# Performance work log

Measured on AMD Instinct MI355X. Metric: run time of the kernel, lower is better.

Reference implementation:

```python
import math
import jax, jax.numpy as jnp
import numpy as np

# ---- config (from ModelConfig) ----
HIDDEN = 2880
HEAD_DIM = 64
N_HEADS = 64
N_KV = 8
Q_MULT = N_HEADS // N_KV  # 8
SLIDING_WINDOW = 128      # left context; causal windowed attention
ROPE_BASE = 150000.0
ROPE_SCALE = 32.0
NTK_ALPHA = 1.0
NTK_BETA = 32.0
INIT_CTX = 4096
RMS_EPS = 1e-5
SM_SCALE = 1.0 / math.sqrt(HEAD_DIM)
Q_DIM = N_HEADS * HEAD_DIM   # 4096
KV_DIM = N_KV * HEAD_DIM     # 512
QKV_DIM = Q_DIM + 2 * KV_DIM # 5120
B, T = 1, 2048


def _rope_cos_sin(n_tokens):
    """YaRN-scaled rotary cache, per RotaryEmbedding._compute_concentration_and_inv_freq."""
    d_half = HEAD_DIM // 2
    freq = ROPE_BASE ** (jnp.arange(0, HEAD_DIM, 2, dtype=jnp.float32) / HEAD_DIM)
    concentration = 0.1 * math.log(ROPE_SCALE) + 1.0
    low = d_half * math.log(INIT_CTX / (NTK_BETA * 2 * math.pi)) / math.log(ROPE_BASE)
    high = d_half * math.log(INIT_CTX / (NTK_ALPHA * 2 * math.pi)) / math.log(ROPE_BASE)
    interpolation = 1.0 / (ROPE_SCALE * freq)
    extrapolation = 1.0 / freq
    ramp = (jnp.arange(d_half, dtype=jnp.float32) - low) / (high - low)
    mask = 1.0 - jnp.clip(ramp, 0.0, 1.0)
    inv_freq = interpolation * (1.0 - mask) + extrapolation * mask
    pos = jnp.arange(n_tokens, dtype=jnp.float32)
    angles = pos[:, None] * inv_freq[None, :]  # [t, d/2]
    return jnp.cos(angles) * concentration, jnp.sin(angles) * concentration


def _apply_rope(x, cos, sin):
    """Interleaved RoPE (matches _apply_rotary_emb). x: [b, t, ..., d]."""
    shape = x.shape
    n_mid = x.ndim - 3  # dims between token axis and feature axis
    c = cos.reshape((1, shape[1]) + (1,) * n_mid + (shape[-1] // 2,))
    s = sin.reshape((1, shape[1]) + (1,) * n_mid + (shape[-1] // 2,))
    x1 = x[..., ::2]
    x2 = x[..., 1::2]
    o1 = x1 * c - x2 * s
    o2 = x2 * c + x1 * s
    return jnp.stack((o1, o2), axis=-1).reshape(shape)


def _rmsnorm(x, scale):
    t = x.astype(jnp.float32)
    t = t * jax.lax.rsqrt(jnp.mean(t * t, axis=-1, keepdims=True) + RMS_EPS)
    return (t * scale).astype(x.dtype)


def setup_inputs() -> dict:
    key = jax.random.key(0)
    ks = jax.random.split(key, 7)
    x = jax.random.normal(ks[0], (B, T, HIDDEN), dtype=jnp.float32)
    norm_scale = jnp.ones((HIDDEN,), dtype=jnp.float32)
    w_qkv = jax.random.normal(ks[1], (QKV_DIM, HIDDEN), dtype=jnp.float32) * (HIDDEN ** -0.5)
    b_qkv = jax.random.normal(ks[2], (QKV_DIM,), dtype=jnp.float32) * 0.02
    sinks = jax.random.normal(ks[3], (N_HEADS,), dtype=jnp.float32)
    w_out = jax.random.normal(ks[4], (HIDDEN, Q_DIM), dtype=jnp.float32) * (Q_DIM ** -0.5)
    b_out = jax.random.normal(ks[5], (HIDDEN,), dtype=jnp.float32) * 0.02
    return {"x": x, "norm_scale": norm_scale, "w_qkv": w_qkv, "b_qkv": b_qkv,
            "sinks": sinks, "w_out": w_out, "b_out": b_out}


def reference(x, norm_scale, w_qkv, b_qkv, sinks, w_out, b_out):
    b, t, _ = x.shape
    h = _rmsnorm(x, norm_scale)
    qkv = h @ w_qkv.T + b_qkv  # [b, t, 5120]
    q = qkv[..., :Q_DIM].reshape(b, t, N_KV, Q_MULT, HEAD_DIM)
    k = qkv[..., Q_DIM:Q_DIM + KV_DIM].reshape(b, t, N_KV, HEAD_DIM)
    v = qkv[..., Q_DIM + KV_DIM:].reshape(b, t, N_KV, HEAD_DIM)

    cos, sin = _rope_cos_sin(t)
    q = _apply_rope(q, cos, sin)
    k = _apply_rope(k, cos, sin)

    # sliding-window causal attention with sink logits (sdpa windowed path)
    left_ctx = SLIDING_WINDOW
    window = left_ctx + 1
    kp = jnp.pad(k, ((0, 0), (left_ctx, 0), (0, 0), (0, 0)))
    vp = jnp.pad(v, ((0, 0), (left_ctx, 0), (0, 0), (0, 0)))
    gather_idx = jnp.arange(t)[:, None] + jnp.arange(window)[None, :]  # into padded axis
    kwin = kp[:, gather_idx]  # [b, t, w, n_kv, d]
    vwin = vp[:, gather_idx]

    pos = jnp.arange(t)[:, None] + (jnp.arange(window) - left_ctx)[None, :]
    valid = (pos >= 0) & (pos < t)  # [t, w]

    scores = jnp.einsum('bthqd,btwhd->bthqw', q, kwin).astype(jnp.float32) * SM_SCALE
    scores = jnp.where(valid[None, :, None, None, :], scores, -jnp.inf)

    sink = (sinks * math.log(2.0)).reshape(N_KV, Q_MULT)
    sink = jnp.broadcast_to(sink[None, None, :, :, None], (b, t, N_KV, Q_MULT, 1))
    scores = jnp.concatenate([scores, sink], axis=-1)  # [b, t, h, q, w+1]

    w_attn = jax.nn.softmax(scores, axis=-1)[..., :-1].astype(v.dtype)
    attn = jnp.einsum('bthqw,btwhd->bthqd', w_attn, vwin).reshape(b, t, -1)

    out = attn @ w_out.T + b_out
    return x + out
```

## Files before the change

### kernel.cpp

```cpp
#include <hip/hip_runtime.h>
#include <math.h>

typedef unsigned short u16;
typedef unsigned int   u32;
using f32x4  = __attribute__((ext_vector_type(4))) float;
using bf16x8 = __attribute__((ext_vector_type(8))) __bf16;

#define HIDDEN   2880
#define QKVD     5120
#define QD       4096
#define TTOK     2048
#define NKV      8
#define QMULT    8
#define HD       64
#define NPAD     2944

#define PREP_QKV_BLOCKS  14400
#define PREP_RMS_BLOCKS  2048

static __device__ __forceinline__ float bflo(u32 u){ return __uint_as_float(u << 16); }
static __device__ __forceinline__ float bfhi(u32 u){ return __uint_as_float(u & 0xffff0000u); }
static __device__ __forceinline__ u16 f2bf(float f){
    u32 u = __float_as_uint(f);
    u32 r = (u + 0x7fffu + ((u >> 16) & 1u)) >> 16;
    return (u16)r;
}

static __device__ __forceinline__ void glds16(const void* g, void* l) {
    __builtin_amdgcn_global_load_lds(
        (__attribute__((address_space(1))) void*)g,
        (__attribute__((address_space(3))) void*)l,
        16, 0, 0);
}

#define BAR() asm volatile("s_barrier" ::: "memory")

__global__ __launch_bounds__(256) void prep_kernel(const float* __restrict__ w_qkv,
                                                   u16* __restrict__ wqkv_bf,
                                                   const float* __restrict__ x,
                                                   const float* __restrict__ scale,
                                                   u16* __restrict__ h) {
    const int b = blockIdx.x;
    const int tid = threadIdx.x;
    if (b < PREP_QKV_BLOCKS) {
        int i = b * 256 + tid;
        float4 f = ((const float4*)w_qkv)[i];
        ushort4 o;
        o.x = f2bf(f.x); o.y = f2bf(f.y); o.z = f2bf(f.z); o.w = f2bf(f.w);
        ((ushort4*)wqkv_bf)[i] = o;
    } else {
        const int t = b - PREP_QKV_BLOCKS;
        const float4* xr = (const float4*)(x + (long)t * HIDDEN);
        float4 v[3];
        float ss = 0.f;
        #pragma unroll
        for (int it = 0; it < 3; ++it) {
            int i4 = tid + it * 256;
            if (i4 < 720) {
                v[it] = xr[i4];
                ss += v[it].x*v[it].x + v[it].y*v[it].y + v[it].z*v[it].z + v[it].w*v[it].w;
            }
        }
        #pragma unroll
        for (int off = 32; off > 0; off >>= 1) ss += __shfl_down(ss, off);
        __shared__ float red[4];
        if ((tid & 63) == 0) red[tid >> 6] = ss;
        __syncthreads();
        float tot = red[0] + red[1] + red[2] + red[3];
        float rr = rsqrtf(tot * (1.0f / HIDDEN) + 1e-5f);
        ushort4* hr = (ushort4*)(h + (long)t * HIDDEN);
        #pragma unroll
        for (int it = 0; it < 3; ++it) {
            int i4 = tid + it * 256;
            if (i4 < 720) {
                float4 s4 = ((const float4*)scale)[i4];
                ushort4 o;
                o.x = f2bf(v[it].x * rr * s4.x);
                o.y = f2bf(v[it].y * rr * s4.y);
                o.z = f2bf(v[it].z * rr * s4.z);
                o.w = f2bf(v[it].w * rr * s4.w);
                hr[i4] = o;
            }
        }
    }
}


#define READ_BQ(SET, BASE, NQ) do { \
    SET[0][0] = *(const bf16x8*)((BASE) + (2*(NQ)+0)*2048 + off0); \
    SET[0][1] = *(const bf16x8*)((BASE) + (2*(NQ)+0)*2048 + off1); \
    SET[1][0] = *(const bf16x8*)((BASE) + (2*(NQ)+1)*2048 + off0); \
    SET[1][1] = *(const bf16x8*)((BASE) + (2*(NQ)+1)*2048 + off1); \
} while (0)

#define READ_AQ(BASE) do { \
    _Pragma("unroll") \
    for (int mi_ = 0; mi_ < 4; ++mi_) { \
        aq[mi_][0] = *(const bf16x8*)((BASE) + mi_*2048 + off0); \
        aq[mi_][1] = *(const bf16x8*)((BASE) + mi_*2048 + off1); \
    } \
} while (0)

#define MFMA_N(NQ, SET) do { \
    __builtin_amdgcn_s_setprio(1); \
    _Pragma("unroll") \
    for (int mi_ = 0; mi_ < 4; ++mi_) { \
        _Pragma("unroll") \
        for (int j_ = 0; j_ < 2; ++j_) { \
            acc[mi_][2*(NQ)+j_] = __builtin_amdgcn_mfma_f32_16x16x32_bf16(aq[mi_][0], SET[j_][0], acc[mi_][2*(NQ)+j_], 0, 0, 0); \
            acc[mi_][2*(NQ)+j_] = __builtin_amdgcn_mfma_f32_16x16x32_bf16(aq[mi_][1], SET[j_][1], acc[mi_][2*(NQ)+j_], 0, 0, 0); \
        } \
    } \
    __builtin_amdgcn_s_setprio(0); \
} while (0)

__global__ __launch_bounds__(512, 2) void gemm_bt_8ph(const u16* __restrict__ A,
                                                      const u16* __restrict__ B,
                                                      u16* __restrict__ C0,
                                                      int N, int K, int ksplit,
                                                      int blimit, int colmax,
                                                      int nz_gemm,
                                                      const float* __restrict__ wout_src,
                                                      u16* __restrict__ wout_dst) {
    const int tid  = threadIdx.x;

    if ((int)blockIdx.z >= nz_gemm) {
        const long nb = (long)gridDim.x * gridDim.y;
        long bidx = (long)blockIdx.y * gridDim.x + blockIdx.x;
        long i = bidx * 512 + tid;
        const long tot = (long)NPAD * QD / 4;
        const long stride = nb * 512;
        for (; i < tot; i += stride) {
            long idx = i * 4;
            int row = (int)(idx >> 12);
            int col = (int)(idx & 4095);
            ushort4 o;
            if (row < HIDDEN) {
                float4 f = *(const float4*)(wout_src + (long)row * QD + col);
                o.x = f2bf(f.x); o.y = f2bf(f.y); o.z = f2bf(f.z); o.w = f2bf(f.w);
            } else {
                o.x = 0; o.y = 0; o.z = 0; o.w = 0;
            }
            ((ushort4*)wout_dst)[i] = o;
        }
        return;
    }

    extern __shared__ u16 smem[];
    u16* const smA = smem;
    u16* const smB = smem + 2 * 256 * 64;
    const int lane = tid & 63;
    const int wv   = tid >> 6;
    const int wm2  = wv >> 1;
    const int wn2  = wv & 1;
    const long m0  = (long)blockIdx.y * 256;
    const long n0  = (long)blockIdx.x * 256;
    const int kbase = blockIdx.z * ksplit;
    int krem = K - kbase; if (krem > ksplit) krem = ksplit;
    const int NT   = krem >> 6;
    u16* C = C0 + (size_t)blockIdx.z * ((size_t)TTOK * N);

    const int srow = tid >> 3;
    const int sg8  = ((tid & 7) ^ (srow & 7)) << 3;
    const int fr   = lane & 15;
    const int off0 = ((lane >> 4) << 4) ^ ((lane & 7) << 4);
    const int off1 = off0 ^ 64;
    const char* aR = (const char*)smA + (wm2 * 64  + fr) * 128;
    const char* bR = (const char*)smB + (wn2 * 128 + fr) * 128;

    f32x4 acc[4][8];
    #pragma unroll
    for (int i = 0; i < 4; ++i)
        #pragma unroll
        for (int j = 0; j < 8; ++j) acc[i][j] = f32x4{0.f, 0.f, 0.f, 0.f};

    const u16* Asrc = A + (m0 + srow) * (long)K + kbase + sg8;
    auto stageA = [&](int t) {
        char* dst = (char*)smA + (t & 1) * 32768 + wv * 1024;
        const u16* src = Asrc + t * 64;
        #pragma unroll
        for (int hj = 0; hj < 4; ++hj)
            glds16(src + (size_t)(hj * 64) * K, dst + hj * 8192);
    };
    auto stageBh = [&](int t, int h) {
        char* dst = (char*)smB + (t & 1) * 32768 + (h * 128 + wv * 8) * 128;
        #pragma unroll
        for (int j = 0; j < 2; ++j) {
            long r = n0 + h * 128 + j * 64 + srow;
            if (r > blimit) r = blimit;
            glds16(B + (size_t)r * K + kbase + t * 64 + sg8, dst + j * 8192);
        }
    };

    bf16x8 aq[4][2], bqE[2][2], bqO[2][2];

    stageA(0);
    stageBh(0, 0); stageBh(0, 1);
    if (NT > 1) {
        stageA(1);
        stageBh(1, 0);
        asm volatile("s_waitcnt vmcnt(6)" ::: "memory");
    } else {
        asm volatile("s_waitcnt vmcnt(0)" ::: "memory");
    }
    BAR();
    READ_BQ(bqE, bR, 0);
    READ_AQ(aR);
    BAR();

    for (int t = 0; t < NT; ++t) {
        const char* aS1 = aR + ((t + 1) & 1) * 32768;
        const char* bS  = bR + (t & 1) * 32768;
        const char* bS1 = bR + ((t + 1) & 1) * 32768;
        READ_BQ(bqO, bS, 1);
        if (t + 1 < NT) stageBh(t + 1, 1);
        if (t + 2 < NT) stageA(t + 2);
        MFMA_N(0, bqE);
        BAR();
        READ_BQ(bqE, bS, 2);
        MFMA_N(1, bqO);
        BAR();
        READ_BQ(bqO, bS, 3);
        MFMA_N(2, bqE);
        if (t + 2 < NT)      asm volatile("s_waitcnt vmcnt(4)" ::: "memory");
        else if (t + 1 < NT) asm volatile("s_waitcnt vmcnt(0)" ::: "memory");
        BAR();
        if (t + 1 < NT) READ_BQ(bqE, bS1, 0);
        if (t + 2 < NT) stageBh(t + 2, 0);
        MFMA_N(3, bqO);
        if (t + 1 < NT) READ_AQ(aS1);
        BAR();
    }

    const int cr = (lane >> 4) * 4;
    const int cc = lane & 15;
    #pragma unroll
    for (int nf = 0; nf < 8; ++nf) {
        long col = n0 + wn2 * 128 + nf * 16 + cc;
        if (col < colmax) {
            #pragma unroll
            for (int mi = 0; mi < 4; ++mi) {
                long row = m0 + wm2 * 64 + mi * 16 + cr;
                #pragma unroll
                for (int r2 = 0; r2 < 4; ++r2)
                    C[(row + r2) * (long)N + col] = f2bf(acc[mi][nf][r2]);
            }
        }
    }
}

__global__ __launch_bounds__(256) void rope_kernel(const u16* __restrict__ p1,
                                                   const float* __restrict__ b_qkv,
                                                   u16* __restrict__ qr,
                                                   u16* __restrict__ kr,
                                                   u16* __restrict__ vr,
                                                   int nsplit) {
    const int t = blockIdx.x;
    const int tid = threadIdx.x;
    __shared__ float cs[32], sn[32];
    if (tid < 32) {
        float fi = (float)tid;
        float freq   = exp2f(17.1946032f * (fi * (1.0f / 32.0f)));
        float interp = 1.0f / (32.0f * freq);
        float extra  = 1.0f / freq;
        float ramp   = (fi - 8.0927802f) * (1.0f / (17.3980220f - 8.0927802f));
        float rc     = fminf(fmaxf(ramp, 0.0f), 1.0f);
        float invf   = interp * rc + extra * (1.0f - rc);
        float ang    = (float)t * invf;
        cs[tid] = cosf(ang) * 1.3465736f;
        sn[tid] = sinf(ang) * 1.3465736f;
    }
    __syncthreads();
    const u16* rowA = p1 + (long)t * QKVD;
    auto pair = [&](int col) -> float2 {
        float2 bb = *(const float2*)(b_qkv + col);
        float a = bb.x, b = bb.y;
        for (int s = 0; s < nsplit; ++s) {
            u32 u = *(const u32*)(rowA + (size_t)s * TTOK * QKVD + col);
            a += bflo(u); b += bfhi(u);
        }
        return make_float2(a, b);
    };
    for (int p = tid; p < 2048; p += 256) {
        int hd2 = p >> 5, i = p & 31;
        float2 ab = pair(hd2 * 64 + 2 * i);
        float o1 = ab.x * cs[i] - ab.y * sn[i];
        float o2 = ab.y * cs[i] + ab.x * sn[i];
        *(u32*)(qr + (long)t * QD + hd2 * 64 + 2 * i) = (u32)f2bf(o1) | ((u32)f2bf(o2) << 16);
    }
    {
        int kv = tid >> 5, i = tid & 31;
        float2 ab = pair(QD + kv * 64 + 2 * i);
        float o1 = ab.x * cs[i] - ab.y * sn[i];
        float o2 = ab.y * cs[i] + ab.x * sn[i];
        *(u32*)(kr + ((long)kv * TTOK + t) * HD + 2 * i) = (u32)f2bf(o1) | ((u32)f2bf(o2) << 16);
    }
    {
        int kv = tid >> 5, d2 = tid & 31;
        float2 ab = pair(QD + 512 + kv * 64 + 2 * d2);
        *(u32*)(vr + ((long)kv * TTOK + t) * HD + 2 * d2) = (u32)f2bf(ab.x) | ((u32)f2bf(ab.y) << 16);
    }
}

__global__ __launch_bounds__(256, 2) void attn_kernel(const u16* __restrict__ qr,
                                                      const u16* __restrict__ kr,
                                                      const u16* __restrict__ vr,
                                                      const float* __restrict__ sinks,
                                                      u16* __restrict__ o) {
    const int t0  = blockIdx.x * 16;
    const int h   = blockIdx.y;
    const int qhg = blockIdx.z;
    const int tid = threadIdx.x;
    const int lane = tid & 63, wv = tid >> 6;
    __shared__ __align__(16) u16 ks[144][72];
    __shared__ __align__(16) u16 Vt[64][168];
    __shared__ __align__(16) u16 P [4][16][168];
    const u16* kb = kr + (long)h * TTOK * HD;
    const u16* vb = vr + (long)h * TTOK * HD;

    #pragma unroll
    for (int i = 0; i < 5; ++i) {
        int idx = i * 256 + tid;
        if (idx < 144 * 8) {
            int rr = idx >> 3, c = idx & 7;
            int tk = t0 - 128 + rr;
            int tks = tk < 0 ? 0 : tk;
            *(uint4*)&ks[rr][c * 8] = *(const uint4*)(kb + (long)tks * HD + c * 8);
        }
    }
    #pragma unroll
    for (int c4 = 0; c4 < 8; ++c4) {
        if (tid < 144) {
            int tk = t0 - 128 + tid;
            int tks = tk < 0 ? 0 : tk;
            uint4 v4 = *(const uint4*)(vb + (long)tks * HD + c4 * 8);
            int d0 = c4 * 8;
            Vt[d0+0][tid] = (u16)(v4.x & 0xffff); Vt[d0+1][tid] = (u16)(v4.x >> 16);
            Vt[d0+2][tid] = (u16)(v4.y & 0xffff); Vt[d0+3][tid] = (u16)(v4.y >> 16);
            Vt[d0+4][tid] = (u16)(v4.z & 0xffff); Vt[d0+5][tid] = (u16)(v4.z >> 16);
            Vt[d0+6][tid] = (u16)(v4.w & 0xffff); Vt[d0+7][tid] = (u16)(v4.w >> 16);
        }
    }
    if (tid < 128) {
        *(uint4*)&Vt[tid >> 1][144 + (tid & 1) * 8] = uint4{0, 0, 0, 0};
    }
    if (lane < 32) {
        *(uint4*)&P[wv][lane >> 1][144 + (lane & 1) * 8] = uint4{0, 0, 0, 0};
    }
    __syncthreads();

    const int qh   = qhg * 4 + wv;
    const int head = h * QMULT + qh;
    const int fr = lane & 15, fk = (lane >> 4) * 8;
    const int cr = (lane >> 4) * 4;

    const u16* qrow = qr + (long)(t0 + fr) * QD + head * HD;
    bf16x8 qf0 = *(const bf16x8*)(qrow + fk);
    bf16x8 qf1 = *(const bf16x8*)(qrow + 32 + fk);

    const int kmin = 128 - t0;
    float lsum[4] = {0.f, 0.f, 0.f, 0.f};

    for (int nt = 0; nt < 9; ++nt) {
        bf16x8 b0 = *(const bf16x8*)&ks[nt * 16 + fr][fk];
        bf16x8 b1 = *(const bf16x8*)&ks[nt * 16 + fr][32 + fk];
        f32x4 s = f32x4{0.f, 0.f, 0.f, 0.f};
        s = __builtin_amdgcn_mfma_f32_16x16x32_bf16(qf0, b0, s, 0, 0, 0);
        s = __builtin_amdgcn_mfma_f32_16x16x32_bf16(qf1, b1, s, 0, 0, 0);
        const int kk = nt * 16 + fr;
        #pragma unroll
        for (int r = 0; r < 4; ++r) {
            int row = cr + r;
            bool valid = (kk >= row) && (kk <= row + 128) && (kk >= kmin);
            float p = valid ? __expf(s[r] * 0.125f) : 0.0f;
            lsum[r] += p;
            P[wv][row][kk] = f2bf(p);
        }
    }

    f32x4 oacc[4];
    #pragma unroll
    for (int dt = 0; dt < 4; ++dt) oacc[dt] = f32x4{0.f, 0.f, 0.f, 0.f};
    #pragma unroll
    for (int k5 = 0; k5 < 5; ++k5) {
        const int k0 = k5 * 32;
        bf16x8 pa = *(const bf16x8*)&P[wv][fr][k0 + fk];
        #pragma unroll
        for (int dt = 0; dt < 4; ++dt) {
            bf16x8 vf = *(const bf16x8*)&Vt[dt * 16 + fr][k0 + fk];
            oacc[dt] = __builtin_amdgcn_mfma_f32_16x16x32_bf16(pa, vf, oacc[dt], 0, 0, 0);
        }
    }

    #pragma unroll
    for (int r = 0; r < 4; ++r) {
        float v = lsum[r];
        v += __shfl_xor(v, 1);
        v += __shfl_xor(v, 2);
        v += __shfl_xor(v, 4);
        v += __shfl_xor(v, 8);
        lsum[r] = v;
    }
    const float sk = exp2f(sinks[head]);
    float inv[4];
    #pragma unroll
    for (int r = 0; r < 4; ++r) inv[r] = 1.0f / (lsum[r] + sk);

    #pragma unroll
    for (int dt = 0; dt < 4; ++dt) {
        #pragma unroll
        for (int r = 0; r < 4; ++r) {
            o[(long)(t0 + cr + r) * QD + head * HD + dt * 16 + fr] = f2bf(oacc[dt][r] * inv[r]);
        }
    }
}

__global__ __launch_bounds__(256) void reduce2_kernel(const u16* __restrict__ p2a,
                                                      const u16* __restrict__ p2b,
                                                      const float* __restrict__ x,
                                                      const float* __restrict__ b_out,
                                                      float* __restrict__ out) {
    const int row = blockIdx.y;
    const int c4 = blockIdx.x * 256 + threadIdx.x;
    if (c4 >= 720) return;
    const int col = c4 * 4;
    ushort4 ua = *(const ushort4*)(p2a + (long)row * NPAD + col);
    ushort4 ub = *(const ushort4*)(p2b + (long)row * NPAD + col);
    float4 xv = *(const float4*)(x + (long)row * HIDDEN + col);
    float4 bv = *(const float4*)(b_out + col);
    float4 o;
    o.x = xv.x + bv.x + __uint_as_float((u32)ua.x << 16) + __uint_as_float((u32)ub.x << 16);
    o.y = xv.y + bv.y + __uint_as_float((u32)ua.y << 16) + __uint_as_float((u32)ub.y << 16);
    o.z = xv.z + bv.z + __uint_as_float((u32)ua.z << 16) + __uint_as_float((u32)ub.z << 16);
    o.w = xv.w + bv.w + __uint_as_float((u32)ua.w << 16) + __uint_as_float((u32)ub.w << 16);
    *(float4*)(out + (long)row * HIDDEN + col) = o;
}

extern "C" void kernel_launch(void* const* d_in, const int* in_sizes, int n_in,
                              void* d_out, int out_size, void* d_ws, size_t ws_size,
                              hipStream_t stream) {
    const float* x      = (const float*)d_in[0];
    const float* nscale = (const float*)d_in[1];
    const float* w_qkv  = (const float*)d_in[2];
    const float* b_qkv  = (const float*)d_in[3];
    const float* sinks  = (const float*)d_in[4];
    const float* w_out  = (const float*)d_in[5];
    const float* b_out  = (const float*)d_in[6];
    float* out = (float*)d_out;

    static int smem_set = 0;
    if (!smem_set) {
        hipFuncSetAttribute((const void*)gemm_bt_8ph,
                            hipFuncAttributeMaxDynamicSharedMemorySize, 131072);
        smem_set = 1;
    }

    const size_t slab = (size_t)TTOK * QKVD * 2;
    const size_t fixed = ((size_t)QKVD * HIDDEN * 2)
                       + ((size_t)NPAD * QD * 2)
                       + ((size_t)TTOK * HIDDEN * 2)
                       + ((size_t)TTOK * QD * 2)
                       + 4096;
    const int gs1 = (fixed + 3 * slab <= ws_size) ? 3 : 2;

    char* ws = (char*)d_ws;
    size_t off = 0;
    auto alloc = [&](size_t bytes) { void* p = ws + off; off += (bytes + 255) & ~(size_t)255; return p; };
    u16* wqkv_bf = (u16*)alloc((size_t)QKVD * HIDDEN * 2);
    u16* wout_bf = (u16*)alloc((size_t)NPAD * QD * 2);
    u16* h       = (u16*)alloc((size_t)TTOK * HIDDEN * 2);
    u16* p1      = (u16*)alloc((size_t)gs1 * slab);
    u16* qrot    = (u16*)alloc((size_t)TTOK * QD * 2);
    u16* attn = wqkv_bf;
    u16* krot = wqkv_bf + (size_t)TTOK * QD;
    u16* vrot = krot + (size_t)NKV * TTOK * HD;
    u16* p2   = p1;

    prep_kernel<<<PREP_QKV_BLOCKS + PREP_RMS_BLOCKS, 256, 0, stream>>>(
        w_qkv, wqkv_bf, x, nscale, h);
    const int ks1 = (gs1 == 3) ? (HIDDEN / 3) : 1472;
    gemm_bt_8ph<<<dim3(QKVD / 256, TTOK / 256, gs1 + 1), 512, 131072, stream>>>(
        h, wqkv_bf, p1, QKVD, HIDDEN, ks1, QKVD - 1, QKVD, gs1, w_out, wout_bf);
    rope_kernel<<<TTOK, 256, 0, stream>>>(p1, b_qkv, qrot, krot, vrot, gs1);
    attn_kernel<<<dim3(TTOK / 16, NKV, 2), 256, 0, stream>>>(qrot, krot, vrot, sinks, attn);
    gemm_bt_8ph<<<dim3((NPAD + 255) / 256, TTOK / 256, 2), 512, 131072, stream>>>(
        attn, wout_bf, p2, NPAD, QD, QD / 2, NPAD - 1, NPAD, 2, nullptr, nullptr);
    reduce2_kernel<<<dim3(3, TTOK), 256, 0, stream>>>(
        p2, p2 + (size_t)TTOK * NPAD, x, b_out, out);
}
```

Before: 355.9 us.

## Drop mid-iteration GEMM barriers and remove split-K from QKV projection

Inside the main GEMM loop, two of the four workgroup barriers per iteration become compiler scheduling barriers. Explicit lgkmcnt and vmcnt waits wrapped in sched_barrier keep the remaining LDS and global-load ordering correct. The QKV projection now runs without split-K (one K slice, grid z of 2 covering the GEMM and the w_out conversion), so the partial-sum slabs and their reduction in rope go away. The trade-off is fewer workgroups in the QKV GEMM and a longer K loop per block, and the removed barriers rely on the double-buffer layout to avoid LDS hazards.

```diff
diff --git a/kernel.cpp b/kernel.cpp
--- a/kernel.cpp
+++ b/kernel.cpp
@@ -33,7 +33,10 @@
         16, 0, 0);
 }
 
-#define BAR() asm volatile("s_barrier" ::: "memory")
+#define SB0()   __builtin_amdgcn_sched_barrier(0)
+#define BARB()  do { SB0(); __builtin_amdgcn_s_barrier(); SB0(); } while (0)
+#define LGKM0() do { asm volatile("s_waitcnt lgkmcnt(0)"); SB0(); } while (0)
+#define VMW(N)  do { SB0(); asm volatile("s_waitcnt vmcnt(" #N ")"); SB0(); } while (0)
 
 __global__ __launch_bounds__(256) void prep_kernel(const float* __restrict__ w_qkv,
                                                    u16* __restrict__ wqkv_bf,
@@ -199,14 +202,15 @@
     if (NT > 1) {
         stageA(1);
         stageBh(1, 0);
-        asm volatile("s_waitcnt vmcnt(6)" ::: "memory");
+        VMW(6);
     } else {
-        asm volatile("s_waitcnt vmcnt(0)" ::: "memory");
-    }
-    BAR();
+        VMW(0);
+    }
+    BARB();
     READ_BQ(bqE, bR, 0);
     READ_AQ(aR);
-    BAR();
+    LGKM0();
+    BARB();
 
     for (int t = 0; t < NT; ++t) {
         const char* aS1 = aR + ((t + 1) & 1) * 32768;
@@ -216,20 +220,21 @@
         if (t + 1 < NT) stageBh(t + 1, 1);
         if (t + 2 < NT) stageA(t + 2);
         MFMA_N(0, bqE);
-        BAR();
+        SB0();
         READ_BQ(bqE, bS, 2);
         MFMA_N(1, bqO);
-        BAR();
+        SB0();
         READ_BQ(bqO, bS, 3);
         MFMA_N(2, bqE);
-        if (t + 2 < NT)      asm volatile("s_waitcnt vmcnt(4)" ::: "memory");
-        else if (t + 1 < NT) asm volatile("s_waitcnt vmcnt(0)" ::: "memory");
-        BAR();
+        if (t + 2 < NT)      VMW(4);
+        else if (t + 1 < NT) VMW(0);
+        BARB();
         if (t + 1 < NT) READ_BQ(bqE, bS1, 0);
         if (t + 2 < NT) stageBh(t + 2, 0);
         MFMA_N(3, bqO);
         if (t + 1 < NT) READ_AQ(aS1);
-        BAR();
+        LGKM0();
+        BARB();
     }
 
     const int cr = (lane >> 4) * 4;
@@ -455,21 +460,15 @@
         smem_set = 1;
     }
 
-    const size_t slab = (size_t)TTOK * QKVD * 2;
-    const size_t fixed = ((size_t)QKVD * HIDDEN * 2)
-                       + ((size_t)NPAD * QD * 2)
-                       + ((size_t)TTOK * HIDDEN * 2)
-                       + ((size_t)TTOK * QD * 2)
-                       + 4096;
-    const int gs1 = (fixed + 3 * slab <= ws_size) ? 3 : 2;
-
     char* ws = (char*)d_ws;
     size_t off = 0;
     auto alloc = [&](size_t bytes) { void* p = ws + off; off += (bytes + 255) & ~(size_t)255; return p; };
+    const size_t p1_bytes  = (size_t)TTOK * QKVD * 2;
+    const size_t p2_bytes  = (size_t)2 * TTOK * NPAD * 2;
     u16* wqkv_bf = (u16*)alloc((size_t)QKVD * HIDDEN * 2);
     u16* wout_bf = (u16*)alloc((size_t)NPAD * QD * 2);
     u16* h       = (u16*)alloc((size_t)TTOK * HIDDEN * 2);
-    u16* p1      = (u16*)alloc((size_t)gs1 * slab);
+    u16* p1      = (u16*)alloc(p1_bytes > p2_bytes ? p1_bytes : p2_bytes);
     u16* qrot    = (u16*)alloc((size_t)TTOK * QD * 2);
     u16* attn = wqkv_bf;
     u16* krot = wqkv_bf + (size_t)TTOK * QD;
@@ -478,10 +477,9 @@
 
     prep_kernel<<<PREP_QKV_BLOCKS + PREP_RMS_BLOCKS, 256, 0, stream>>>(
         w_qkv, wqkv_bf, x, nscale, h);
-    const int ks1 = (gs1 == 3) ? (HIDDEN / 3) : 1472;
-    gemm_bt_8ph<<<dim3(QKVD / 256, TTOK / 256, gs1 + 1), 512, 131072, stream>>>(
-        h, wqkv_bf, p1, QKVD, HIDDEN, ks1, QKVD - 1, QKVD, gs1, w_out, wout_bf);
-    rope_kernel<<<TTOK, 256, 0, stream>>>(p1, b_qkv, qrot, krot, vrot, gs1);
+    gemm_bt_8ph<<<dim3(QKVD / 256, TTOK / 256, 2), 512, 131072, stream>>>(
+        h, wqkv_bf, p1, QKVD, HIDDEN, HIDDEN, QKVD - 1, QKVD, 1, w_out, wout_bf);
+    rope_kernel<<<TTOK, 256, 0, stream>>>(p1, b_qkv, qrot, krot, vrot, 1);
     attn_kernel<<<dim3(TTOK / 16, NKV, 2), 256, 0, stream>>>(qrot, krot, vrot, sinks, attn);
     gemm_bt_8ph<<<dim3((NPAD + 255) / 256, TTOK / 256, 2), 512, 131072, stream>>>(
         attn, wout_bf, p2, NPAD, QD, QD / 2, NPAD - 1, NPAD, 2, nullptr, nullptr);
```

New measurement: 323.4 us. 9.1% less time.
